# Kernel tuning notes

Hardware: AMD Instinct MI355X
Metric: run time of the kernel (lower is better)

## Reference

```python
import jax, jax.numpy as jnp
import numpy as np

EMPTY_IDX = 6  # relabeling of the original -1 ('EMPTY') expert to row 6 of the stacked tables


def setup_inputs() -> dict:
    key = jax.random.key(0)
    k1, k2, k3, k4, k5, k6 = jax.random.split(key, 6)
    B, L, H, T, E = 32, 2048, 768, 12, 7
    return {
        "sequence_output": jax.random.normal(k1, (B, L, H), dtype=jnp.float32),
        "module_net_w": jax.random.normal(k2, (E, H, H), dtype=jnp.float32),
        "span_net_w": jax.random.normal(k3, (E, H, 2), dtype=jnp.float32),
        "turns": jax.random.randint(k4, (B, T, 2), 0, L),
        "key_phrase_span": jax.random.randint(k5, (B, T, 2), 0, L),
        "module_index": jax.random.randint(k6, (B, T), 0, E),
    }


def reference(sequence_output, module_net_w, span_net_w, turns, key_phrase_span, module_index):
    seq = sequence_output            # [B, L, H]
    B, L, H = seq.shape
    T = turns.shape[1]
    f32 = seq.dtype

    eidx = module_index              # [B, T], 0..6 (6 == EMPTY, original -1)
    mod_mask = (eidx != EMPTY_IDX).astype(f32)            # module_index != -1
    start_pos = turns[:, :, 0]       # [B, T] turn start token positions
    turns_mask = (start_pos >= 0).astype(f32)             # turns[:,:,0] != -1

    # context_hidden_step = sequence_output[arange(B), start] for every step
    ctx = jnp.take_along_axis(seq, start_pos[:, :, None], axis=1)   # [B, T, H]

    # einsum('bh,bhz,blz->blz'): (ctx @ W_expert) broadcast-multiplied with seq.
    # Compute ctx @ W for ALL experts (tables are tiny), then gather per (b, t).
    cW_all = jnp.einsum('bth,ehz->btez', ctx, module_net_w)         # [B, T, 7, H]
    gidx = jnp.broadcast_to(eidx[:, :, None, None], (B, T, 1, H))
    cW = jnp.take_along_axis(cW_all, gidx, axis=2).squeeze(2)       # [B, T, H]

    span_w = span_net_w[eidx]        # [B, T, H, 2] per-sample expert span weights
    # logits[b,t,l,k] = sum_z seq[b,l,z] * cW[b,t,z] * span_w[b,t,z,k]
    v = cW[..., None] * span_w                                      # [B, T, H, 2]
    logits = jnp.einsum('blz,btzk->btlk', seq, v)                   # [B, T, L, 2]

    # CrossEntropyLoss(ignore_index=-1, reduction='none') over the L axis
    logsm = jax.nn.log_softmax(logits, axis=2)                      # [B, T, L, 2]
    tgt = key_phrase_span[:, :, :T][:, :T]  # [B, T, 2]
    tgt = key_phrase_span
    safe = jnp.clip(tgt, 0, L - 1)                                  # [B, T, 2]
    picked = jnp.take_along_axis(logsm, safe[:, :, None, :], axis=2).squeeze(2)  # [B, T, 2]
    ce = jnp.where(tgt >= 0, -picked, jnp.zeros((), f32))           # [B, T, 2]
    step_loss = 0.5 * (ce[..., 0] + ce[..., 1]) * mod_mask          # [B, T]

    loss = (step_loss * turns_mask).sum() / turns_mask.sum()
    return loss
```

## Files before the change

### kernel.cpp

```cpp
#include <hip/hip_runtime.h>
#include <math.h>

#define Bz 32
#define Lz 2048
#define Hz 768
#define Tz 12
#define Ez 7
#define EMPTYIDX 6
#define NCOL 24
#define LCHUNK 128
#define NCHUNK 16

#define K1A_ZC 3
#define K1A_HB 48
#define K1A_HC 16
__global__ void k1a_cw(const float* __restrict__ seq, const float* __restrict__ W,
                       const int* __restrict__ turns, const int* __restrict__ midx,
                       float* __restrict__ cW) {
    int bx = blockIdx.x;
    int e  = bx % Ez;
    int zc = (bx / Ez) % K1A_ZC;
    int hc = bx / (Ez * K1A_ZC);
    int z  = zc * 256 + threadIdx.x;
    int h0 = hc * K1A_HB;
    int tid = threadIdx.x;

    __shared__ int itemsS[Bz * Tz];
    __shared__ int cntS;
    if (tid == 0) cntS = 0;
    __syncthreads();
    for (int i = tid; i < Bz * Tz; i += 256) {
        int ei = midx[i];
        ei = min(max(ei, 0), Ez - 1);
        if (ei == e) {
            int p = atomicAdd(&cntS, 1);
            itemsS[p] = i;
        }
    }
    __syncthreads();
    int cnt = cntS;

    const float* Wb = W + ((size_t)e * Hz + h0) * Hz + z;
    float w[K1A_HB];
#pragma unroll
    for (int j = 0; j < K1A_HB; ++j) w[j] = Wb[(size_t)j * Hz];

    for (int n = 0; n < cnt; ++n) {
        int i  = itemsS[n];
        int b  = i / Tz;
        int st = turns[2 * i];
        st = min(max(st, 0), Lz - 1);
        const float* c = seq + ((size_t)(b * Lz + st)) * Hz + h0;
        float acc = 0.f;
#pragma unroll
        for (int j = 0; j < K1A_HB; ++j) acc = fmaf(c[j], w[j], acc);
        atomicAdd(&cW[(size_t)i * Hz + z], acc);
    }
}

__global__ void k1b_v(const float* __restrict__ cW, const float* __restrict__ spanw,
                      const int* __restrict__ midx, float* __restrict__ v) {
    int idx = blockIdx.x * 256 + threadIdx.x;
    int i = idx / Hz;
    int z = idx - i * Hz;
    int e = midx[i];
    e = min(max(e, 0), Ez - 1);
    float cw = cW[idx];
    int b = i / Tz, t = i - b * Tz;
    size_t vb = ((size_t)(b * NCOL + t * 2)) * Hz + z;
    v[vb]      = cw * spanw[(e * Hz + z) * 2 + 0];
    v[vb + Hz] = cw * spanw[(e * Hz + z) * 2 + 1];
}

#define BK 64
#define ATS (BK + 4)
#define K2_T 128
__global__ void __launch_bounds__(K2_T, 2)
k2_logits(const float* __restrict__ seq, const float* __restrict__ v,
          float* __restrict__ pm, float* __restrict__ ps) {
    int bx = blockIdx.x;
    int b  = bx / NCHUNK;
    int ch = bx % NCHUNK;
    int l0 = ch * LCHUNK;
    int tid = threadIdx.x;
    int rg   = tid >> 2;
    int colg = tid & 3;
    __shared__ float at[LCHUNK][ATS];
    __shared__ float vt[NCOL][ATS];
    __shared__ float red_m[NCOL][33];
    __shared__ float red_s[NCOL][33];
    float acc[4][6];
#pragma unroll
    for (int r = 0; r < 4; ++r)
#pragma unroll
        for (int j = 0; j < 6; ++j) acc[r][j] = 0.f;

    const float* A = seq + ((size_t)b * Lz + l0) * Hz;
    const float* V = v + (size_t)b * NCOL * Hz;

    float4 ra[16];
    float4 rv[3];
#pragma unroll
    for (int p = 0; p < 16; ++p) {
        int j = tid + p * K2_T, r = j >> 4, c4 = j & 15;
        ra[p] = *(const float4*)&A[(size_t)r * Hz + c4 * 4];
    }
#pragma unroll
    for (int p = 0; p < 3; ++p) {
        int j = tid + p * K2_T, c = j >> 4, q = j & 15;
        rv[p] = *(const float4*)&V[(size_t)c * Hz + q * 4];
    }

    for (int k0 = 0; k0 < Hz; k0 += BK) {
#pragma unroll
        for (int p = 0; p < 16; ++p) {
            int j = tid + p * K2_T, r = j >> 4, c4 = j & 15;
            *(float4*)&at[r][c4 * 4] = ra[p];
        }
#pragma unroll
        for (int p = 0; p < 3; ++p) {
            int j = tid + p * K2_T, c = j >> 4, q = j & 15;
            *(float4*)&vt[c][q * 4] = rv[p];
        }
        __syncthreads();
        if (k0 + BK < Hz) {
#pragma unroll
            for (int p = 0; p < 16; ++p) {
                int j = tid + p * K2_T, r = j >> 4, c4 = j & 15;
                ra[p] = *(const float4*)&A[(size_t)r * Hz + k0 + BK + c4 * 4];
            }
#pragma unroll
            for (int p = 0; p < 3; ++p) {
                int j = tid + p * K2_T, c = j >> 4, q = j & 15;
                rv[p] = *(const float4*)&V[(size_t)c * Hz + k0 + BK + q * 4];
            }
        }
#pragma unroll
        for (int kk = 0; kk < BK; kk += 4) {
            float4 a0 = *(const float4*)&at[rg +  0][kk];
            float4 a1 = *(const float4*)&at[rg + 32][kk];
            float4 a2 = *(const float4*)&at[rg + 64][kk];
            float4 a3 = *(const float4*)&at[rg + 96][kk];
            float4 v0 = *(const float4*)&vt[colg * 6 + 0][kk];
            float4 v1 = *(const float4*)&vt[colg * 6 + 1][kk];
            float4 v2 = *(const float4*)&vt[colg * 6 + 2][kk];
            float4 v3 = *(const float4*)&vt[colg * 6 + 3][kk];
            float4 v4 = *(const float4*)&vt[colg * 6 + 4][kk];
            float4 v5 = *(const float4*)&vt[colg * 6 + 5][kk];
#define DOT(ACC, AV, VV) ACC = fmaf(AV.w, VV.w, fmaf(AV.z, VV.z, fmaf(AV.y, VV.y, fmaf(AV.x, VV.x, ACC))))
#define ROW(r, AV) \
            DOT(acc[r][0], AV, v0); DOT(acc[r][1], AV, v1); DOT(acc[r][2], AV, v2); \
            DOT(acc[r][3], AV, v3); DOT(acc[r][4], AV, v4); DOT(acc[r][5], AV, v5);
            ROW(0, a0) ROW(1, a1) ROW(2, a2) ROW(3, a3)
#undef ROW
#undef DOT
        }
        __syncthreads();
    }
#pragma unroll
    for (int j = 0; j < 6; ++j) {
        int c = colg * 6 + j;
        float m = fmaxf(fmaxf(acc[0][j], acc[1][j]), fmaxf(acc[2][j], acc[3][j]));
        float s = expf(acc[0][j] - m) + expf(acc[1][j] - m) +
                  expf(acc[2][j] - m) + expf(acc[3][j] - m);
        red_m[c][rg] = m;
        red_s[c][rg] = s;
    }
    __syncthreads();
    if (tid < NCOL) {
        int c = tid;
        float m = red_m[c][0];
        for (int r = 1; r < 32; ++r) m = fmaxf(m, red_m[c][r]);
        float s = 0.f;
        for (int r = 0; r < 32; ++r) s += red_s[c][r] * expf(red_m[c][r] - m);
        pm[((size_t)b * NCOL + c) * NCHUNK + ch] = m;
        ps[((size_t)b * NCOL + c) * NCHUNK + ch] = s;
    }
}

__global__ void k3_picked(const float* __restrict__ seq, const float* __restrict__ v,
                          const int* __restrict__ kps, float* __restrict__ picked) {
    int i = blockIdx.x;
    int b = i / Tz, t = i % Tz;
    int lane = threadIdx.x;
    for (int k = 0; k < 2; ++k) {
        int tgt  = kps[2 * i + k];
        int safe = min(max(tgt, 0), Lz - 1);
        const float* srow = seq + ((size_t)b * Lz + safe) * Hz;
        const float* vcol = v + ((size_t)(b * NCOL + t * 2 + k)) * Hz;
        float sum = 0.f;
#pragma unroll
        for (int q = 0; q < Hz / 64; ++q) {
            int z = lane + q * 64;
            sum = fmaf(srow[z], vcol[z], sum);
        }
        for (int o = 32; o > 0; o >>= 1) sum += __shfl_down(sum, o, 64);
        if (lane == 0) picked[b * NCOL + t * 2 + k] = sum;
    }
}

__global__ void k4_final(const int* __restrict__ midx, const int* __restrict__ turns,
                         const int* __restrict__ kps,
                         const float* __restrict__ pm, const float* __restrict__ ps,
                         const float* __restrict__ picked, float* __restrict__ out) {
    int tid = threadIdx.x;
    int i = tid;
    int b = i / Tz, t = i % Tz;
    int e = midx[i];
    float modm  = (e != EMPTYIDX) ? 1.f : 0.f;
    float tmask = (turns[2 * i] >= 0) ? 1.f : 0.f;
    float ce[2];
#pragma unroll
    for (int k = 0; k < 2; ++k) {
        int c = t * 2 + k;
        const float* pmr = pm + ((size_t)b * NCOL + c) * NCHUNK;
        const float* psr = ps + ((size_t)b * NCOL + c) * NCHUNK;
        float m = pmr[0];
        for (int chn = 1; chn < NCHUNK; ++chn) m = fmaxf(m, pmr[chn]);
        float s = 0.f;
        for (int chn = 0; chn < NCHUNK; ++chn) s += psr[chn] * expf(pmr[chn] - m);
        float lse = m + logf(s);
        int tgt = kps[2 * i + k];
        ce[k] = (tgt >= 0) ? (lse - picked[b * NCOL + c]) : 0.f;
    }
    float contrib = 0.5f * (ce[0] + ce[1]) * modm * tmask;

    __shared__ float wsum[6], wmask[6];
    float sl = contrib, sm = tmask;
    for (int o = 32; o > 0; o >>= 1) {
        sl += __shfl_down(sl, o, 64);
        sm += __shfl_down(sm, o, 64);
    }
    int w = tid >> 6, lane = tid & 63;
    if (lane == 0) { wsum[w] = sl; wmask[w] = sm; }
    __syncthreads();
    if (tid == 0) {
        float a = 0.f, mk = 0.f;
        for (int ww = 0; ww < 6; ++ww) { a += wsum[ww]; mk += wmask[ww]; }
        out[0] = a / mk;
    }
}

extern "C" void kernel_launch(void* const* d_in, const int* in_sizes, int n_in,
                              void* d_out, int out_size, void* d_ws, size_t ws_size,
                              hipStream_t stream) {
    const float* seq   = (const float*)d_in[0];
    const float* W     = (const float*)d_in[1];
    const float* spanw = (const float*)d_in[2];
    const int*   turns = (const int*)d_in[3];
    const int*   kps   = (const int*)d_in[4];
    const int*   midx  = (const int*)d_in[5];
    float* out = (float*)d_out;

    char* ws = (char*)d_ws;
    float* cW     = (float*)(ws + 0);
    float* v      = (float*)(ws + 1179648);
    float* pm     = (float*)(ws + 1179648 + 2359296);
    float* ps     = (float*)(ws + 1179648 + 2359296 + 49152);
    float* picked = (float*)(ws + 1179648 + 2359296 + 98304);

    hipMemsetAsync(cW, 0, (size_t)384 * Hz * sizeof(float), stream);
    hipLaunchKernelGGL(k1a_cw, dim3(Ez * K1A_ZC * K1A_HC), dim3(256), 0, stream,
                       seq, W, turns, midx, cW);
    hipLaunchKernelGGL(k1b_v, dim3((384 * Hz) / 256), dim3(256), 0, stream,
                       cW, spanw, midx, v);
    hipLaunchKernelGGL(k2_logits, dim3(Bz * NCHUNK), dim3(K2_T), 0, stream, seq, v, pm, ps);
    hipLaunchKernelGGL(k3_picked, dim3(Bz * Tz), dim3(64), 0, stream, seq, v, kps, picked);
    hipLaunchKernelGGL(k4_final, dim3(1), dim3(Bz * Tz), 0, stream,
                       midx, turns, kps, pm, ps, picked, out);
}
```

Measured before the change: 420.5 us.

## Use direct global-to-LDS loads with XOR-swizzled double-buffered tiles in logits GEMM

```diff
diff --git a/kernel.cpp b/kernel.cpp
--- a/kernel.cpp
+++ b/kernel.cpp
@@ -73,9 +73,17 @@
 }
 
 #define BK 64
-#define ATS (BK + 4)
 #define K2_T 128
-__global__ void __launch_bounds__(K2_T, 2)
+#define ACH 2048
+#define VCH 384
+
+__device__ __forceinline__ void gl_lds16(const float* g, float4* l) {
+    __builtin_amdgcn_global_load_lds(
+        (const __attribute__((address_space(1))) void*)g,
+        (__attribute__((address_space(3))) void*)l, 16, 0, 0);
+}
+
+__global__ void __launch_bounds__(K2_T, 1)
 k2_logits(const float* __restrict__ seq, const float* __restrict__ v,
           float* __restrict__ pm, float* __restrict__ ps) {
     int bx = blockIdx.x;
@@ -85,10 +93,9 @@
     int tid = threadIdx.x;
     int rg   = tid >> 2;
     int colg = tid & 3;
-    __shared__ float at[LCHUNK][ATS];
-    __shared__ float vt[NCOL][ATS];
-    __shared__ float red_m[NCOL][33];
-    __shared__ float red_s[NCOL][33];
+
+    __shared__ float4 lds[2][ACH + VCH];
+
     float acc[4][6];
 #pragma unroll
     for (int r = 0; r < 4; ++r)
@@ -98,55 +105,51 @@
     const float* A = seq + ((size_t)b * Lz + l0) * Hz;
     const float* V = v + (size_t)b * NCOL * Hz;
 
-    float4 ra[16];
-    float4 rv[3];
-#pragma unroll
-    for (int p = 0; p < 16; ++p) {
-        int j = tid + p * K2_T, r = j >> 4, c4 = j & 15;
-        ra[p] = *(const float4*)&A[(size_t)r * Hz + c4 * 4];
-    }
-#pragma unroll
-    for (int p = 0; p < 3; ++p) {
-        int j = tid + p * K2_T, c = j >> 4, q = j & 15;
-        rv[p] = *(const float4*)&V[(size_t)c * Hz + q * 4];
-    }
-
-    for (int k0 = 0; k0 < Hz; k0 += BK) {
-#pragma unroll
-        for (int p = 0; p < 16; ++p) {
-            int j = tid + p * K2_T, r = j >> 4, c4 = j & 15;
-            *(float4*)&at[r][c4 * 4] = ra[p];
-        }
-#pragma unroll
-        for (int p = 0; p < 3; ++p) {
-            int j = tid + p * K2_T, c = j >> 4, q = j & 15;
-            *(float4*)&vt[c][q * 4] = rv[p];
-        }
+#define DMA_TILE(pb, k0)                                                     \
+    {                                                                        \
+        float4* atb = &lds[pb][0];                                           \
+        float4* vtb = &lds[pb][ACH];                                         \
+        _Pragma("unroll")                                                    \
+        for (int p = 0; p < 16; ++p) {                                       \
+            int c = p * K2_T + tid;                                          \
+            int r = c >> 4;                                                  \
+            int q = (c & 15) ^ (r & 15);                                     \
+            gl_lds16(&A[(size_t)r * Hz + (k0) + q * 4], atb + c);            \
+        }                                                                    \
+        _Pragma("unroll")                                                    \
+        for (int p = 0; p < 3; ++p) {                                        \
+            int c = p * K2_T + tid;                                          \
+            int r = c >> 4;                                                  \
+            int q = (c & 15) ^ (r & 15);                                     \
+            gl_lds16(&V[(size_t)r * Hz + (k0) + q * 4], vtb + c);            \
+        }                                                                    \
+    }
+
+    DMA_TILE(0, 0)
+
+    int rx = rg & 15;
+    int cr0 = colg * 6;
+    for (int t = 0; t < Hz / BK; ++t) {
         __syncthreads();
-        if (k0 + BK < Hz) {
-#pragma unroll
-            for (int p = 0; p < 16; ++p) {
-                int j = tid + p * K2_T, r = j >> 4, c4 = j & 15;
-                ra[p] = *(const float4*)&A[(size_t)r * Hz + k0 + BK + c4 * 4];
-            }
-#pragma unroll
-            for (int p = 0; p < 3; ++p) {
-                int j = tid + p * K2_T, c = j >> 4, q = j & 15;
-                rv[p] = *(const float4*)&V[(size_t)c * Hz + k0 + BK + q * 4];
-            }
-        }
-#pragma unroll
-        for (int kk = 0; kk < BK; kk += 4) {
-            float4 a0 = *(const float4*)&at[rg +  0][kk];
-            float4 a1 = *(const float4*)&at[rg + 32][kk];
-            float4 a2 = *(const float4*)&at[rg + 64][kk];
-            float4 a3 = *(const float4*)&at[rg + 96][kk];
-            float4 v0 = *(const float4*)&vt[colg * 6 + 0][kk];
-            float4 v1 = *(const float4*)&vt[colg * 6 + 1][kk];
-            float4 v2 = *(const float4*)&vt[colg * 6 + 2][kk];
-            float4 v3 = *(const float4*)&vt[colg * 6 + 3][kk];
-            float4 v4 = *(const float4*)&vt[colg * 6 + 4][kk];
-            float4 v5 = *(const float4*)&vt[colg * 6 + 5][kk];
+        if (t + 1 < Hz / BK) {
+            int nb = (t + 1) & 1;
+            int nk = (t + 1) * BK;
+            if (nb) { DMA_TILE(1, nk) } else { DMA_TILE(0, nk) }
+        }
+        const float4* at4 = &lds[t & 1][0];
+        const float4* vt4 = &lds[t & 1][ACH];
+#pragma unroll
+        for (int q = 0; q < 16; ++q) {
+            float4 a0 = at4[(rg +  0) * 16 + (q ^ rx)];
+            float4 a1 = at4[(rg + 32) * 16 + (q ^ rx)];
+            float4 a2 = at4[(rg + 64) * 16 + (q ^ rx)];
+            float4 a3 = at4[(rg + 96) * 16 + (q ^ rx)];
+            float4 v0 = vt4[(cr0 + 0) * 16 + (q ^ ((cr0 + 0) & 15))];
+            float4 v1 = vt4[(cr0 + 1) * 16 + (q ^ ((cr0 + 1) & 15))];
+            float4 v2 = vt4[(cr0 + 2) * 16 + (q ^ ((cr0 + 2) & 15))];
+            float4 v3 = vt4[(cr0 + 3) * 16 + (q ^ ((cr0 + 3) & 15))];
+            float4 v4 = vt4[(cr0 + 4) * 16 + (q ^ ((cr0 + 4) & 15))];
+            float4 v5 = vt4[(cr0 + 5) * 16 + (q ^ ((cr0 + 5) & 15))];
 #define DOT(ACC, AV, VV) ACC = fmaf(AV.w, VV.w, fmaf(AV.z, VV.z, fmaf(AV.y, VV.y, fmaf(AV.x, VV.x, ACC))))
 #define ROW(r, AV) \
             DOT(acc[r][0], AV, v0); DOT(acc[r][1], AV, v1); DOT(acc[r][2], AV, v2); \
@@ -155,24 +158,26 @@
 #undef ROW
 #undef DOT
         }
-        __syncthreads();
-    }
+    }
+    __syncthreads();
+    float* red_m = (float*)&lds[0][0];
+    float* red_s = red_m + NCOL * 33;
 #pragma unroll
     for (int j = 0; j < 6; ++j) {
-        int c = colg * 6 + j;
+        int c = cr0 + j;
         float m = fmaxf(fmaxf(acc[0][j], acc[1][j]), fmaxf(acc[2][j], acc[3][j]));
         float s = expf(acc[0][j] - m) + expf(acc[1][j] - m) +
                   expf(acc[2][j] - m) + expf(acc[3][j] - m);
-        red_m[c][rg] = m;
-        red_s[c][rg] = s;
+        red_m[c * 33 + rg] = m;
+        red_s[c * 33 + rg] = s;
     }
     __syncthreads();
     if (tid < NCOL) {
         int c = tid;
-        float m = red_m[c][0];
-        for (int r = 1; r < 32; ++r) m = fmaxf(m, red_m[c][r]);
+        float m = red_m[c * 33];
+        for (int r = 1; r < 32; ++r) m = fmaxf(m, red_m[c * 33 + r]);
         float s = 0.f;
-        for (int r = 0; r < 32; ++r) s += red_s[c][r] * expf(red_m[c][r] - m);
+        for (int r = 0; r < 32; ++r) s += red_s[c * 33 + r] * expf(red_m[c * 33 + r] - m);
         pm[((size_t)b * NCOL + c) * NCHUNK + ch] = m;
         ps[((size_t)b * NCOL + c) * NCHUNK + ch] = s;
     }
```

Measured after the change: 375.5 us. 10.7% less time.
